# Performance work log

Measured on AMD Instinct MI355X. Metric: run time of the kernel, lower is better.

The kernel has to match this reference:

```python
import jax, jax.numpy as jnp
import numpy as np

D_MODEL = 256
NHEAD = 8
DK = D_MODEL // NHEAD
EDGE_FEAT_DIM = 7
N_NODES = 2048
N_EDGES = 65536
LN_EPS = 1e-5


def _ln(x, g, b):
    mu = jnp.mean(x, axis=-1, keepdims=True)
    var = jnp.mean(jnp.square(x - mu), axis=-1, keepdims=True)
    return (x - mu) * jax.lax.rsqrt(var + LN_EPS) * g + b


def setup_inputs() -> dict:
    key = jax.random.key(0)
    ks = jax.random.split(key, 16)
    d, h2 = D_MODEL, 2 * D_MODEL
    s = 0.02
    inp = {
        "h": jax.random.normal(ks[0], (N_NODES, d), jnp.float32),
        "edge_attr": jax.random.normal(ks[1], (N_EDGES, EDGE_FEAT_DIM), jnp.float32),
        # weights stored as (in, out): y = x @ W + b (matches torch Linear math)
        "Wq": s * jax.random.normal(ks[2], (d, d), jnp.float32),
        "bq": jnp.zeros((d,), jnp.float32),
        "Wk": s * jax.random.normal(ks[3], (d, d), jnp.float32),
        "bk": jnp.zeros((d,), jnp.float32),
        "Wv": s * jax.random.normal(ks[4], (d, d), jnp.float32),
        "bv": jnp.zeros((d,), jnp.float32),
        "Wo": s * jax.random.normal(ks[5], (d, d), jnp.float32),
        "bo": jnp.zeros((d,), jnp.float32),
        "We": s * jax.random.normal(ks[6], (EDGE_FEAT_DIM, NHEAD), jnp.float32),
        "be": jnp.zeros((NHEAD,), jnp.float32),
        "ln1_g": jnp.ones((d,), jnp.float32),
        "ln1_b": jnp.zeros((d,), jnp.float32),
        "fln_g": jnp.ones((d,), jnp.float32),
        "fln_b": jnp.zeros((d,), jnp.float32),
        "W1": s * jax.random.normal(ks[7], (d, h2), jnp.float32),
        "b1": jnp.zeros((h2,), jnp.float32),
        "W2": s * jax.random.normal(ks[8], (h2, d), jnp.float32),
        "b2": jnp.zeros((d,), jnp.float32),
        "edge_index": jax.random.randint(ks[9], (2, N_EDGES), 0, N_NODES, jnp.int64 if jax.config.jax_enable_x64 else jnp.int32),
    }
    return inp


def reference(h, edge_attr, Wq, bq, Wk, bk, Wv, bv, Wo, bo, We, be,
              ln1_g, ln1_b, fln_g, fln_b, W1, b1, W2, b2, edge_index):
    N = h.shape[0]
    res = h
    # edge bias scattered into dense (N, N, H) tensor
    eb = edge_attr @ We + be                                  # (E, H)
    attn_bias = jnp.zeros((N, N, NHEAD), h.dtype).at[edge_index[0], edge_index[1]].set(eb)
    Q = (h @ Wq + bq).reshape(N, NHEAD, DK)
    K = (h @ Wk + bk).reshape(N, NHEAD, DK)
    V = (h @ Wv + bv).reshape(N, NHEAD, DK)
    scores = jnp.einsum('nhd,mhd->nmh', Q, K) / jnp.sqrt(jnp.float32(DK)) + attn_bias
    attn = jax.nn.softmax(scores, axis=1)                     # softmax over keys m
    out = jnp.einsum('nmh,mhd->nhd', attn, V).reshape(N, D_MODEL)
    out = out @ Wo + bo
    h1 = _ln(res + out, ln1_g, ln1_b)
    ffn = jax.nn.gelu(_ln(h1, fln_g, fln_b) @ W1 + b1, approximate=False) @ W2 + b2
    return h1 + ffn
```

## Files before the change

### kernel.cpp

```cpp
#include <hip/hip_runtime.h>
#include <math.h>

#define NN 2048
#define NE 65536
#define DM 256
#define NH 8
#define DKH 32
#define CAP 128
#define TM2 128
#define SPLIT 4

typedef __attribute__((ext_vector_type(8))) short bf16x8;
typedef __attribute__((ext_vector_type(4))) float f32x4;

#define WAVE_LDS_SYNC() __asm__ volatile("s_waitcnt lgkmcnt(0)" ::: "memory")

__device__ __forceinline__ unsigned short f2b(float f) {
    unsigned u = __float_as_uint(f);
    unsigned r = (u + 0x7FFFu + ((u >> 16) & 1u)) >> 16;
    return (unsigned short)r;
}
__device__ __forceinline__ float b2f(unsigned short s) {
    return __uint_as_float(((unsigned)s) << 16);
}

__global__ __launch_bounds__(256) void prep_all_kernel(
    const float* __restrict__ h, const float* __restrict__ Wq,
    const float* __restrict__ Wk, const float* __restrict__ Wv,
    const float* __restrict__ Wo, const float* __restrict__ W1,
    const float* __restrict__ W2, const float* __restrict__ ea,
    const float* __restrict__ We, const float* __restrict__ be,
    const int* __restrict__ ei,
    unsigned short* __restrict__ hb, unsigned short* __restrict__ Wqkvt,
    unsigned short* __restrict__ Wot, unsigned short* __restrict__ W1t,
    unsigned short* __restrict__ W2t, float* __restrict__ eb,
    int* __restrict__ cnt, int* __restrict__ lst)
{
    int b = blockIdx.x;
    if (b < 4096) {
        int i = b * 256 + threadIdx.x;
        if (i < 524288) {
            hb[i] = f2b(h[i]);
        } else if (i < 720896) {
            int j = i - 524288;
            int n = j >> 8, k = j & 255;
            const float* W = (n < 256) ? Wq : (n < 512) ? Wk : Wv;
            Wqkvt[j] = f2b(W[k * 256 + (n & 255)]);
        } else if (i < 786432) {
            int j = i - 720896;
            int n = j >> 8, k = j & 255;
            Wot[j] = f2b(Wo[k * 256 + n]);
        } else if (i < 917504) {
            int j = i - 786432;
            int n = j >> 8, k = j & 255;
            W1t[j] = f2b(W1[(size_t)k * 512 + n]);
        } else {
            int j = i - 917504;
            int n = j >> 9, k = j & 511;
            W2t[j] = f2b(W2[(size_t)k * 256 + n]);
        }
    } else {
        int e = (b - 4096) * 256 + threadIdx.x;
        float acc[NH];
#pragma unroll
        for (int hh = 0; hh < NH; ++hh) acc[hh] = be[hh];
#pragma unroll
        for (int f = 0; f < 7; ++f) {
            float x = ea[e * 7 + f];
#pragma unroll
            for (int hh = 0; hh < NH; ++hh) acc[hh] = fmaf(x, We[f * NH + hh], acc[hh]);
        }
#pragma unroll
        for (int hh = 0; hh < NH; ++hh)
            eb[e * NH + hh] = acc[hh] * 1.44269504088896f;
        int s = ei[e];
        int p = atomicAdd(&cnt[s], 1);
        if (p < CAP) lst[s * CAP + p] = e;
    }
}

__global__ __launch_bounds__(128) void rowprep_kernel(
    const int* __restrict__ ei, const int* __restrict__ cnt,
    const int* __restrict__ lst, int* __restrict__ sortedDest,
    int* __restrict__ sortedE, int* __restrict__ rowOff)
{
    __shared__ int ds[CAP], es[CAP];
    __shared__ int bc[16], off[17];
    int n = blockIdx.x, t = threadIdx.x;
    int c = cnt[n]; if (c > CAP) c = CAP;
    if (t < 16) bc[t] = 0;
    int e = -1, d = -1;
    if (t < c) { e = lst[n * CAP + t]; d = ei[NE + e]; }
    ds[t] = d; es[t] = e;
    __syncthreads();
    bool win = (t < c);
    if (win) {
        for (int j = 0; j < c; ++j)
            if (ds[j] == d && es[j] > e) { win = false; break; }
    }
    int bkt = (d >= 0) ? (d >> 7) : 0;
    int pos = -1;
    if (win) pos = atomicAdd(&bc[bkt], 1);
    __syncthreads();
    if (t == 0) {
        int s = 0;
        for (int i = 0; i < 16; ++i) { off[i] = s; s += bc[i]; }
        off[16] = s;
    }
    __syncthreads();
    if (win) {
        int p = off[bkt] + pos;
        sortedDest[n * CAP + p] = d;
        sortedE[n * CAP + p] = e;
    }
    if (t < 17) rowOff[n * 17 + t] = off[t];
}

template <int EPI, int MT>
__global__ __launch_bounds__(MT * 4) void gemm_bf16(
    const unsigned short* __restrict__ A, const unsigned short* __restrict__ Bt,
    const float* __restrict__ bias0, const float* __restrict__ bias1,
    const float* __restrict__ bias2, const float* __restrict__ resid,
    void* __restrict__ out0, void* __restrict__ out1, void* __restrict__ out2,
    int M, int N, int K)
{
    __shared__ __align__(16) unsigned short As[MT][136];
    __shared__ __align__(16) unsigned short Bs[64][136];
    int tid = threadIdx.x;
    int wv = tid >> 6, l = tid & 63, l15 = l & 15, quad = l >> 4;
    int m0 = blockIdx.y * MT, n0 = blockIdx.x * 64;

    f32x4 acc[4];
#pragma unroll
    for (int i = 0; i < 4; ++i) acc[i] = (f32x4){0.f, 0.f, 0.f, 0.f};

    for (int k0 = 0; k0 < K; k0 += 128) {
        if (MT == 64) {
            int row = tid >> 2, cb = (tid & 3) * 32;
            const unsigned short* ap = A + (size_t)(m0 + row) * K + k0 + cb;
#pragma unroll
            for (int i = 0; i < 4; ++i)
                *(uint4*)&As[row][cb + i * 8] = *(const uint4*)(ap + i * 8);
            const unsigned short* bp = Bt + (size_t)(n0 + row) * K + k0 + cb;
#pragma unroll
            for (int i = 0; i < 4; ++i)
                *(uint4*)&Bs[row][cb + i * 8] = *(const uint4*)(bp + i * 8);
        } else {
            int rowa = tid >> 2, cba = (tid & 3) * 32;
            const unsigned short* ap = A + (size_t)(m0 + rowa) * K + k0 + cba;
#pragma unroll
            for (int i = 0; i < 4; ++i)
                *(uint4*)&As[rowa][cba + i * 8] = *(const uint4*)(ap + i * 8);
            int rowb = tid >> 1, cbb = (tid & 1) * 64;
            const unsigned short* bp = Bt + (size_t)(n0 + rowb) * K + k0 + cbb;
#pragma unroll
            for (int i = 0; i < 8; ++i)
                *(uint4*)&Bs[rowb][cbb + i * 8] = *(const uint4*)(bp + i * 8);
        }
        __syncthreads();
#pragma unroll
        for (int ks = 0; ks < 4; ++ks) {
            bf16x8 a = *(const bf16x8*)&As[wv * 16 + l15][ks * 32 + quad * 8];
#pragma unroll
            for (int nt = 0; nt < 4; ++nt) {
                bf16x8 b = *(const bf16x8*)&Bs[nt * 16 + l15][ks * 32 + quad * 8];
                acc[nt] = __builtin_amdgcn_mfma_f32_16x16x32_bf16(a, b, acc[nt], 0, 0, 0);
            }
        }
        __syncthreads();
    }

#pragma unroll
    for (int nt = 0; nt < 4; ++nt) {
        int colb = n0 + nt * 16;
        if (EPI == 2 && colb >= 512) {
            int n = colb + l15 - 512;
            float bv = bias2[n];
            unsigned short s0 = f2b(acc[nt][0] + bv);
            unsigned short s1 = f2b(acc[nt][1] + bv);
            unsigned short s2 = f2b(acc[nt][2] + bv);
            unsigned short s3 = f2b(acc[nt][3] + bv);
            uint2 pk = { (unsigned)s0 | ((unsigned)s1 << 16),
                         (unsigned)s2 | ((unsigned)s3 << 16) };
            *(uint2*)((unsigned short*)out2 + (size_t)n * NN + m0 + wv * 16 + quad * 4) = pk;
            continue;
        }
#pragma unroll
        for (int r = 0; r < 4; ++r) {
            int row = m0 + wv * 16 + quad * 4 + r;
            int col = colb + l15;
            float v = acc[nt][r];
            if (EPI == 0) {
                v += bias0[col];
                if (resid) v += resid[(size_t)row * N + col];
                ((float*)out0)[(size_t)row * N + col] = v;
            } else if (EPI == 1) {
                v += bias0[col];
                v = 0.5f * v * (1.0f + erff(v * 0.70710678118654752f));
                ((unsigned short*)out0)[(size_t)row * N + col] = f2b(v);
            } else {
                if (col < 256) {
                    v = (v + bias0[col]) * 0.2550348592f;
                    ((unsigned short*)out0)[(size_t)row * 256 + col] = f2b(v);
                } else {
                    v += bias1[col - 256];
                    ((unsigned short*)out1)[(size_t)row * 256 + col - 256] = f2b(v);
                }
            }
        }
    }
}

__global__ __launch_bounds__(256) void attn_mfma(
    const unsigned short* __restrict__ Qb, const unsigned short* __restrict__ Kb,
    const unsigned short* __restrict__ Vt, const float* __restrict__ eb,
    const int* __restrict__ sortedDest, const int* __restrict__ sortedE,
    const int* __restrict__ rowOff,
    float* __restrict__ accD, float* __restrict__ lD)
{
    __shared__ __align__(16) unsigned short Ks[TM2][40];
    __shared__ __align__(16) unsigned short Vs[32][TM2 + 8];
    __shared__ __align__(16) unsigned short Pn[4][16][TM2 + 16];
    __shared__ float ldelta[4][16];
    int h = blockIdx.y, tid = threadIdx.x;
    int wv = tid >> 6, l = tid & 63, l15 = l & 15, quad = l >> 4;
    int n0 = blockIdx.x * 64 + wv * 16;
    int mz = blockIdx.z;

    if (l < 16) ldelta[wv][l] = 0.f;

    bf16x8 aq = *(const bf16x8*)(Qb + (size_t)(n0 + l15) * DM + h * 32 + quad * 8);

    f32x4 oacc[2];
    oacc[0] = (f32x4){0.f, 0.f, 0.f, 0.f};
    oacc[1] = (f32x4){0.f, 0.f, 0.f, 0.f};
    float lacc = 0.f;
    const unsigned short* Vth = Vt + (size_t)h * 32 * NN;

    int r16 = l >> 2, sub = l & 3;
    int frow = n0 + r16;

    for (int t = 0; t < NN / (TM2 * SPLIT); ++t) {
        int m0 = (mz * (NN / SPLIT)) + t * TM2;
        int ti = m0 >> 7;
        {
            int r = tid >> 1, kc = (tid & 1) * 16;
            const unsigned short* ks = Kb + (size_t)(m0 + r) * DM + h * 32 + kc;
            *(uint4*)&Ks[r][kc]     = *(const uint4*)(ks);
            *(uint4*)&Ks[r][kc + 8] = *(const uint4*)(ks + 8);
            int d = tid >> 3, mc = (tid & 7) * 16;
            const unsigned short* vs = Vth + (size_t)d * NN + m0 + mc;
            *(uint4*)&Vs[d][mc]     = *(const uint4*)(vs);
            *(uint4*)&Vs[d][mc + 8] = *(const uint4*)(vs + 8);
        }
        __syncthreads();
#pragma unroll
        for (int mt = 0; mt < TM2 / 16; ++mt) {
            bf16x8 ak = *(const bf16x8*)&Ks[mt * 16 + l15][quad * 8];
            f32x4 s = __builtin_amdgcn_mfma_f32_16x16x32_bf16(
                ak, aq, (f32x4){0.f, 0.f, 0.f, 0.f}, 0, 0, 0);
            float p0 = __builtin_amdgcn_exp2f(s[0]);
            float p1 = __builtin_amdgcn_exp2f(s[1]);
            float p2 = __builtin_amdgcn_exp2f(s[2]);
            float p3 = __builtin_amdgcn_exp2f(s[3]);
            lacc += (p0 + p1) + (p2 + p3);
            unsigned u0 = (unsigned)f2b(p0) | ((unsigned)f2b(p1) << 16);
            unsigned u1 = (unsigned)f2b(p2) | ((unsigned)f2b(p3) << 16);
            *(uint2*)&Pn[wv][l15][mt * 16 + quad * 4] = (uint2){u0, u1};
        }
        WAVE_LDS_SYNC();
        {
            int o0 = rowOff[frow * 17 + ti];
            int o1 = rowOff[frow * 17 + ti + 1];
            for (int idx = o0 + sub; idx < o1; idx += 4) {
                int d = sortedDest[frow * CAP + idx] - m0;
                int e = sortedE[frow * CAP + idx];
                float expb = __builtin_amdgcn_exp2f(eb[e * NH + h]);
                float pold = b2f(Pn[wv][r16][d]);
                Pn[wv][r16][d] = f2b(pold * expb);
                atomicAdd(&ldelta[wv][r16], pold * (expb - 1.0f));
            }
        }
        WAVE_LDS_SYNC();
#pragma unroll
        for (int kc = 0; kc < TM2 / 32; ++kc) {
            bf16x8 ap = *(const bf16x8*)&Pn[wv][l15][kc * 32 + quad * 8];
#pragma unroll
            for (int nt = 0; nt < 2; ++nt) {
                bf16x8 bv = *(const bf16x8*)&Vs[nt * 16 + l15][kc * 32 + quad * 8];
                oacc[nt] = __builtin_amdgcn_mfma_f32_16x16x32_bf16(ap, bv, oacc[nt], 0, 0, 0);
            }
        }
        __syncthreads();
    }

    lacc += __shfl_xor(lacc, 16);
    lacc += __shfl_xor(lacc, 32);
    float* lDp = lD + (size_t)mz * NN * NH;
    if (l < 16)
        lDp[(size_t)(n0 + l) * NH + h] = lacc + ldelta[wv][l];
    float* aDp = accD + (size_t)mz * NN * DM;
#pragma unroll
    for (int nt = 0; nt < 2; ++nt)
#pragma unroll
        for (int r = 0; r < 4; ++r)
            aDp[(size_t)(n0 + quad * 4 + r) * DM + h * 32 + nt * 16 + l15] = oacc[nt][r];
}

__global__ __launch_bounds__(256) void wo_ln_kernel(
    const float* __restrict__ accD, const float* __restrict__ lD,
    const unsigned short* __restrict__ Wot, const float* __restrict__ bo,
    const float* __restrict__ h, const float* __restrict__ g1,
    const float* __restrict__ b1, const float* __restrict__ g2,
    const float* __restrict__ b2, float* __restrict__ H1,
    unsigned short* __restrict__ X2b)
{
    __shared__ float linv[16][8];
    __shared__ __align__(16) unsigned short As[16][264];
    __shared__ __align__(16) unsigned short Bs[256][40];
    __shared__ float Tt[16][264];
    __shared__ unsigned short X2s[16][264];
    int tid = threadIdx.x, m0 = blockIdx.x * 16;
    int wv = tid >> 6, l = tid & 63, l15 = l & 15, quad = l >> 4;

    if (tid < 128) {
        int r = tid >> 3, hh = tid & 7;
        float ls = 0.f;
#pragma unroll
        for (int s = 0; s < SPLIT; ++s)
            ls += lD[(size_t)s * NN * NH + (size_t)(m0 + r) * NH + hh];
        linv[r][hh] = 1.0f / ls;
    }
    __syncthreads();
#pragma unroll
    for (int ch = 0; ch < 16; ++ch) {
        float o = 0.f;
#pragma unroll
        for (int s = 0; s < SPLIT; ++s)
            o += accD[(size_t)s * NN * DM + (size_t)(m0 + ch) * DM + tid];
        As[ch][tid] = f2b(o * linv[ch][tid >> 5]);
    }
    __syncthreads();

    f32x4 acc[4];
#pragma unroll
    for (int i = 0; i < 4; ++i) acc[i] = (f32x4){0.f, 0.f, 0.f, 0.f};

    for (int k0 = 0; k0 < 256; k0 += 32) {
#pragma unroll
        for (int ps = 0; ps < 4; ++ps) {
            int row = ps * 64 + (tid >> 2), kk = (tid & 3) * 8;
            *(uint4*)&Bs[row][kk] = *(const uint4*)(Wot + (size_t)row * 256 + k0 + kk);
        }
        __syncthreads();
        bf16x8 a = *(const bf16x8*)&As[l15][k0 + quad * 8];
#pragma unroll
        for (int nt = 0; nt < 4; ++nt) {
            bf16x8 b = *(const bf16x8*)&Bs[wv * 64 + nt * 16 + l15][quad * 8];
            acc[nt] = __builtin_amdgcn_mfma_f32_16x16x32_bf16(a, b, acc[nt], 0, 0, 0);
        }
        __syncthreads();
    }

#pragma unroll
    for (int nt = 0; nt < 4; ++nt)
#pragma unroll
        for (int r = 0; r < 4; ++r) {
            int row = quad * 4 + r, col = wv * 64 + nt * 16 + l15;
            Tt[row][col] = acc[nt][r] + bo[col] + h[(size_t)(m0 + row) * DM + col];
        }
    __syncthreads();

    int rr = tid >> 4, l16 = tid & 15;
    float x[16];
#pragma unroll
    for (int j = 0; j < 16; ++j) x[j] = Tt[rr][l16 + 16 * j];
    float mu = 0.f;
#pragma unroll
    for (int j = 0; j < 16; ++j) mu += x[j];
#pragma unroll
    for (int off = 1; off < 16; off <<= 1) mu += __shfl_xor(mu, off);
    mu *= (1.0f / 256.0f);
    float var = 0.f;
#pragma unroll
    for (int j = 0; j < 16; ++j) { float d = x[j] - mu; var += d * d; }
#pragma unroll
    for (int off = 1; off < 16; off <<= 1) var += __shfl_xor(var, off);
    float rs = rsqrtf(var * (1.0f / 256.0f) + 1e-5f);
    float y[16]; float mu2 = 0.f;
#pragma unroll
    for (int j = 0; j < 16; ++j) {
        int c = l16 + 16 * j;
        y[j] = (x[j] - mu) * rs * g1[c] + b1[c];
        mu2 += y[j];
    }
#pragma unroll
    for (int off = 1; off < 16; off <<= 1) mu2 += __shfl_xor(mu2, off);
    mu2 *= (1.0f / 256.0f);
    float var2 = 0.f;
#pragma unroll
    for (int j = 0; j < 16; ++j) { float d = y[j] - mu2; var2 += d * d; }
#pragma unroll
    for (int off = 1; off < 16; off <<= 1) var2 += __shfl_xor(var2, off);
    float rs2 = rsqrtf(var2 * (1.0f / 256.0f) + 1e-5f);
#pragma unroll
    for (int j = 0; j < 16; ++j) {
        int c = l16 + 16 * j;
        Tt[rr][c] = y[j];
        X2s[rr][c] = f2b((y[j] - mu2) * rs2 * g2[c] + b2[c]);
    }
    __syncthreads();
#pragma unroll
    for (int ch = 0; ch < 16; ++ch) {
        H1[(size_t)(m0 + ch) * DM + tid] = Tt[ch][tid];
        X2b[(size_t)(m0 + ch) * DM + tid] = X2s[ch][tid];
    }
}

extern "C" void kernel_launch(void* const* d_in, const int* in_sizes, int n_in,
                              void* d_out, int out_size, void* d_ws, size_t ws_size,
                              hipStream_t stream)
{
    const float* h    = (const float*)d_in[0];
    const float* ea   = (const float*)d_in[1];
    const float* Wq   = (const float*)d_in[2];
    const float* bq   = (const float*)d_in[3];
    const float* Wk   = (const float*)d_in[4];
    const float* bk   = (const float*)d_in[5];
    const float* Wv   = (const float*)d_in[6];
    const float* bv   = (const float*)d_in[7];
    const float* Wo   = (const float*)d_in[8];
    const float* bo   = (const float*)d_in[9];
    const float* We   = (const float*)d_in[10];
    const float* be   = (const float*)d_in[11];
    const float* ln1g = (const float*)d_in[12];
    const float* ln1b = (const float*)d_in[13];
    const float* flng = (const float*)d_in[14];
    const float* flnb = (const float*)d_in[15];
    const float* W1   = (const float*)d_in[16];
    const float* b1   = (const float*)d_in[17];
    const float* W2   = (const float*)d_in[18];
    const float* b2   = (const float*)d_in[19];
    const int*   ei   = (const int*)d_in[20];
    float* out = (float*)d_out;

    char* p = (char*)d_ws;
    float* eb   = (float*)p;           p += (size_t)NE * NH * 4;
    int*   cnt  = (int*)p;             p += (size_t)NN * 4;
    int*   lst  = (int*)p;             p += (size_t)NN * CAP * 4;
    int*   sD   = (int*)p;             p += (size_t)NN * CAP * 4;
    int*   sE   = (int*)p;             p += (size_t)NN * CAP * 4;
    int*   rOff = (int*)p;             p += (size_t)NN * 17 * 4;
    unsigned short* hb    = (unsigned short*)p; p += (size_t)NN * DM * 2;
    unsigned short* Wqkvt = (unsigned short*)p; p += (size_t)768 * 256 * 2;
    unsigned short* Wot   = (unsigned short*)p; p += (size_t)256 * 256 * 2;
    unsigned short* W1t   = (unsigned short*)p; p += (size_t)512 * 256 * 2;
    unsigned short* W2t   = (unsigned short*)p; p += (size_t)256 * 512 * 2;
    unsigned short* Qb    = (unsigned short*)p; p += (size_t)NN * DM * 2;
    unsigned short* Kb    = (unsigned short*)p; p += (size_t)NN * DM * 2;
    unsigned short* Vt    = (unsigned short*)p; p += (size_t)NN * DM * 2;
    float* accD = (float*)p;           p += (size_t)SPLIT * NN * DM * 4;
    float* lD   = (float*)p;           p += (size_t)SPLIT * NN * NH * 4;
    float* H1   = (float*)p;           p += (size_t)NN * DM * 4;
    unsigned short* X2b   = (unsigned short*)p; p += (size_t)NN * DM * 2;
    unsigned short* F1b   = (unsigned short*)p; p += (size_t)NN * 512 * 2;

    hipMemsetAsync(cnt, 0, (size_t)NN * 4, stream);
    prep_all_kernel<<<4096 + NE / 256, 256, 0, stream>>>(
        h, Wq, Wk, Wv, Wo, W1, W2, ea, We, be, ei,
        hb, Wqkvt, Wot, W1t, W2t, eb, cnt, lst);
    rowprep_kernel<<<NN, 128, 0, stream>>>(ei, cnt, lst, sD, sE, rOff);

    gemm_bf16<2, 64><<<dim3(768 / 64, NN / 64), 256, 0, stream>>>(
        hb, Wqkvt, bq, bk, bv, nullptr, Qb, Kb, Vt, NN, 768, 256);

    attn_mfma<<<dim3(NN / 64, NH, SPLIT), 256, 0, stream>>>(
        Qb, Kb, Vt, eb, sD, sE, rOff, accD, lD);

    wo_ln_kernel<<<NN / 16, 256, 0, stream>>>(
        accD, lD, Wot, bo, h, ln1g, ln1b, flng, flnb, H1, X2b);

    gemm_bf16<1, 64><<<dim3(512 / 64, NN / 64), 256, 0, stream>>>(
        X2b, W1t, b1, nullptr, nullptr, nullptr, F1b, nullptr, nullptr, NN, 512, 256);
    gemm_bf16<0, 32><<<dim3(256 / 64, NN / 32), 128, 0, stream>>>(
        F1b, W2t, b2, nullptr, nullptr, H1, out, nullptr, nullptr, NN, 256, 512);
}
```

Measured before the change: 171.7 us.

## Fuse h bf16 conversion into QKV GEMM and replace LDS atomics with shuffles

Removes the separate h-to-bf16 conversion from the prep kernel. The QKV GEMM now loads fp32 h directly and packs it to bf16 while staging into LDS, which drops one global write plus re-read and halves the prep grid. In the attention kernel, the per-row edge-bias correction was accumulated with LDS atomics; it now uses a per-lane register sum reduced with cross-lane shuffles. A cheaper round-half-up bf16 pack helper (pk2) replaces round-to-nearest-even in several places, which slightly changes rounding behaviour.

```diff
diff --git a/kernel.cpp b/kernel.cpp
--- a/kernel.cpp
+++ b/kernel.cpp
@@ -23,44 +23,44 @@
 __device__ __forceinline__ float b2f(unsigned short s) {
     return __uint_as_float(((unsigned)s) << 16);
 }
+__device__ __forceinline__ unsigned pk2(float a, float b) {
+    unsigned ua = __float_as_uint(a) + 0x8000u;
+    unsigned ub = __float_as_uint(b) + 0x8000u;
+    return (ua >> 16) | (ub & 0xFFFF0000u);
+}
 
 __global__ __launch_bounds__(256) void prep_all_kernel(
-    const float* __restrict__ h, const float* __restrict__ Wq,
-    const float* __restrict__ Wk, const float* __restrict__ Wv,
-    const float* __restrict__ Wo, const float* __restrict__ W1,
-    const float* __restrict__ W2, const float* __restrict__ ea,
-    const float* __restrict__ We, const float* __restrict__ be,
-    const int* __restrict__ ei,
-    unsigned short* __restrict__ hb, unsigned short* __restrict__ Wqkvt,
-    unsigned short* __restrict__ Wot, unsigned short* __restrict__ W1t,
-    unsigned short* __restrict__ W2t, float* __restrict__ eb,
-    int* __restrict__ cnt, int* __restrict__ lst)
+    const float* __restrict__ Wq, const float* __restrict__ Wk,
+    const float* __restrict__ Wv, const float* __restrict__ Wo,
+    const float* __restrict__ W1, const float* __restrict__ W2,
+    const float* __restrict__ ea, const float* __restrict__ We,
+    const float* __restrict__ be, const int* __restrict__ ei,
+    unsigned short* __restrict__ Wqkvt, unsigned short* __restrict__ Wot,
+    unsigned short* __restrict__ W1t, unsigned short* __restrict__ W2t,
+    float* __restrict__ eb, int* __restrict__ cnt, int* __restrict__ lst)
 {
     int b = blockIdx.x;
-    if (b < 4096) {
+    if (b < 2048) {
         int i = b * 256 + threadIdx.x;
-        if (i < 524288) {
-            hb[i] = f2b(h[i]);
-        } else if (i < 720896) {
-            int j = i - 524288;
-            int n = j >> 8, k = j & 255;
+        if (i < 196608) {
+            int n = i >> 8, k = i & 255;
             const float* W = (n < 256) ? Wq : (n < 512) ? Wk : Wv;
-            Wqkvt[j] = f2b(W[k * 256 + (n & 255)]);
-        } else if (i < 786432) {
-            int j = i - 720896;
+            Wqkvt[i] = f2b(W[k * 256 + (n & 255)]);
+        } else if (i < 262144) {
+            int j = i - 196608;
             int n = j >> 8, k = j & 255;
             Wot[j] = f2b(Wo[k * 256 + n]);
-        } else if (i < 917504) {
-            int j = i - 786432;
+        } else if (i < 393216) {
+            int j = i - 262144;
             int n = j >> 8, k = j & 255;
             W1t[j] = f2b(W1[(size_t)k * 512 + n]);
         } else {
-            int j = i - 917504;
+            int j = i - 393216;
             int n = j >> 9, k = j & 511;
             W2t[j] = f2b(W2[(size_t)k * 256 + n]);
         }
     } else {
-        int e = (b - 4096) * 256 + threadIdx.x;
+        int e = (b - 2048) * 256 + threadIdx.x;
         float acc[NH];
 #pragma unroll
         for (int hh = 0; hh < NH; ++hh) acc[hh] = be[hh];
@@ -116,9 +116,9 @@
     if (t < 17) rowOff[n * 17 + t] = off[t];
 }
 
-template <int EPI, int MT>
+template <int EPI, int MT, int AF32>
 __global__ __launch_bounds__(MT * 4) void gemm_bf16(
-    const unsigned short* __restrict__ A, const unsigned short* __restrict__ Bt,
+    const void* __restrict__ Av, const unsigned short* __restrict__ Bt,
     const float* __restrict__ bias0, const float* __restrict__ bias1,
     const float* __restrict__ bias2, const float* __restrict__ resid,
     void* __restrict__ out0, void* __restrict__ out1, void* __restrict__ out2,
@@ -137,17 +137,31 @@
     for (int k0 = 0; k0 < K; k0 += 128) {
         if (MT == 64) {
             int row = tid >> 2, cb = (tid & 3) * 32;
-            const unsigned short* ap = A + (size_t)(m0 + row) * K + k0 + cb;
-#pragma unroll
-            for (int i = 0; i < 4; ++i)
-                *(uint4*)&As[row][cb + i * 8] = *(const uint4*)(ap + i * 8);
+            if (AF32) {
+                const float* ap = (const float*)Av + (size_t)(m0 + row) * K + k0 + cb;
+#pragma unroll
+                for (int i = 0; i < 4; ++i) {
+                    float4 f0 = *(const float4*)(ap + i * 8);
+                    float4 f1 = *(const float4*)(ap + i * 8 + 4);
+                    uint4 pk = { pk2(f0.x, f0.y), pk2(f0.z, f0.w),
+                                 pk2(f1.x, f1.y), pk2(f1.z, f1.w) };
+                    *(uint4*)&As[row][cb + i * 8] = pk;
+                }
+            } else {
+                const unsigned short* ap =
+                    (const unsigned short*)Av + (size_t)(m0 + row) * K + k0 + cb;
+#pragma unroll
+                for (int i = 0; i < 4; ++i)
+                    *(uint4*)&As[row][cb + i * 8] = *(const uint4*)(ap + i * 8);
+            }
             const unsigned short* bp = Bt + (size_t)(n0 + row) * K + k0 + cb;
 #pragma unroll
             for (int i = 0; i < 4; ++i)
                 *(uint4*)&Bs[row][cb + i * 8] = *(const uint4*)(bp + i * 8);
         } else {
             int rowa = tid >> 2, cba = (tid & 3) * 32;
-            const unsigned short* ap = A + (size_t)(m0 + rowa) * K + k0 + cba;
+            const unsigned short* ap =
+                (const unsigned short*)Av + (size_t)(m0 + rowa) * K + k0 + cba;
 #pragma unroll
             for (int i = 0; i < 4; ++i)
                 *(uint4*)&As[rowa][cba + i * 8] = *(const uint4*)(ap + i * 8);
@@ -176,12 +190,8 @@
         if (EPI == 2 && colb >= 512) {
             int n = colb + l15 - 512;
             float bv = bias2[n];
-            unsigned short s0 = f2b(acc[nt][0] + bv);
-            unsigned short s1 = f2b(acc[nt][1] + bv);
-            unsigned short s2 = f2b(acc[nt][2] + bv);
-            unsigned short s3 = f2b(acc[nt][3] + bv);
-            uint2 pk = { (unsigned)s0 | ((unsigned)s1 << 16),
-                         (unsigned)s2 | ((unsigned)s3 << 16) };
+            uint2 pk = { pk2(acc[nt][0] + bv, acc[nt][1] + bv),
+                         pk2(acc[nt][2] + bv, acc[nt][3] + bv) };
             *(uint2*)((unsigned short*)out2 + (size_t)n * NN + m0 + wv * 16 + quad * 4) = pk;
             continue;
         }
@@ -221,20 +231,18 @@
     __shared__ __align__(16) unsigned short Ks[TM2][40];
     __shared__ __align__(16) unsigned short Vs[32][TM2 + 8];
     __shared__ __align__(16) unsigned short Pn[4][16][TM2 + 16];
-    __shared__ float ldelta[4][16];
     int h = blockIdx.y, tid = threadIdx.x;
     int wv = tid >> 6, l = tid & 63, l15 = l & 15, quad = l >> 4;
     int n0 = blockIdx.x * 64 + wv * 16;
     int mz = blockIdx.z;
 
-    if (l < 16) ldelta[wv][l] = 0.f;
-
     bf16x8 aq = *(const bf16x8*)(Qb + (size_t)(n0 + l15) * DM + h * 32 + quad * 8);
 
     f32x4 oacc[2];
     oacc[0] = (f32x4){0.f, 0.f, 0.f, 0.f};
     oacc[1] = (f32x4){0.f, 0.f, 0.f, 0.f};
     float lacc = 0.f;
+    float dreg = 0.f;
     const unsigned short* Vth = Vt + (size_t)h * 32 * NN;
 
     int r16 = l >> 2, sub = l & 3;
@@ -264,9 +272,8 @@
             float p2 = __builtin_amdgcn_exp2f(s[2]);
             float p3 = __builtin_amdgcn_exp2f(s[3]);
             lacc += (p0 + p1) + (p2 + p3);
-            unsigned u0 = (unsigned)f2b(p0) | ((unsigned)f2b(p1) << 16);
-            unsigned u1 = (unsigned)f2b(p2) | ((unsigned)f2b(p3) << 16);
-            *(uint2*)&Pn[wv][l15][mt * 16 + quad * 4] = (uint2){u0, u1};
+            *(uint2*)&Pn[wv][l15][mt * 16 + quad * 4] =
+                (uint2){pk2(p0, p1), pk2(p2, p3)};
         }
         WAVE_LDS_SYNC();
         {
@@ -278,7 +285,7 @@
                 float expb = __builtin_amdgcn_exp2f(eb[e * NH + h]);
                 float pold = b2f(Pn[wv][r16][d]);
                 Pn[wv][r16][d] = f2b(pold * expb);
-                atomicAdd(&ldelta[wv][r16], pold * (expb - 1.0f));
+                dreg += pold * (expb - 1.0f);
             }
         }
         WAVE_LDS_SYNC();
@@ -296,9 +303,12 @@
 
     lacc += __shfl_xor(lacc, 16);
     lacc += __shfl_xor(lacc, 32);
+    dreg += __shfl_xor(dreg, 1);
+    dreg += __shfl_xor(dreg, 2);
+    float dtot = __shfl(dreg, l15 * 4);
     float* lDp = lD + (size_t)mz * NN * NH;
     if (l < 16)
-        lDp[(size_t)(n0 + l) * NH + h] = lacc + ldelta[wv][l];
+        lDp[(size_t)(n0 + l) * NH + h] = lacc + dtot;
     float* aDp = accD + (size_t)mz * NN * DM;
 #pragma unroll
     for (int nt = 0; nt < 2; ++nt)
@@ -451,7 +461,6 @@
     int*   sD   = (int*)p;             p += (size_t)NN * CAP * 4;
     int*   sE   = (int*)p;             p += (size_t)NN * CAP * 4;
     int*   rOff = (int*)p;             p += (size_t)NN * 17 * 4;
-    unsigned short* hb    = (unsigned short*)p; p += (size_t)NN * DM * 2;
     unsigned short* Wqkvt = (unsigned short*)p; p += (size_t)768 * 256 * 2;
     unsigned short* Wot   = (unsigned short*)p; p += (size_t)256 * 256 * 2;
     unsigned short* W1t   = (unsigned short*)p; p += (size_t)512 * 256 * 2;
@@ -466,13 +475,13 @@
     unsigned short* F1b   = (unsigned short*)p; p += (size_t)NN * 512 * 2;
 
     hipMemsetAsync(cnt, 0, (size_t)NN * 4, stream);
-    prep_all_kernel<<<4096 + NE / 256, 256, 0, stream>>>(
-        h, Wq, Wk, Wv, Wo, W1, W2, ea, We, be, ei,
-        hb, Wqkvt, Wot, W1t, W2t, eb, cnt, lst);
+    prep_all_kernel<<<2048 + NE / 256, 256, 0, stream>>>(
+        Wq, Wk, Wv, Wo, W1, W2, ea, We, be, ei,
+        Wqkvt, Wot, W1t, W2t, eb, cnt, lst);
     rowprep_kernel<<<NN, 128, 0, stream>>>(ei, cnt, lst, sD, sE, rOff);
 
-    gemm_bf16<2, 64><<<dim3(768 / 64, NN / 64), 256, 0, stream>>>(
-        hb, Wqkvt, bq, bk, bv, nullptr, Qb, Kb, Vt, NN, 768, 256);
+    gemm_bf16<2, 64, 1><<<dim3(768 / 64, NN / 64), 256, 0, stream>>>(
+        h, Wqkvt, bq, bk, bv, nullptr, Qb, Kb, Vt, NN, 768, 256);
 
     attn_mfma<<<dim3(NN / 64, NH, SPLIT), 256, 0, stream>>>(
         Qb, Kb, Vt, eb, sD, sE, rOff, accD, lD);
@@ -480,8 +489,8 @@
     wo_ln_kernel<<<NN / 16, 256, 0, stream>>>(
         accD, lD, Wot, bo, h, ln1g, ln1b, flng, flnb, H1, X2b);
 
-    gemm_bf16<1, 64><<<dim3(512 / 64, NN / 64), 256, 0, stream>>>(
+    gemm_bf16<1, 64, 0><<<dim3(512 / 64, NN / 64), 256, 0, stream>>>(
         X2b, W1t, b1, nullptr, nullptr, nullptr, F1b, nullptr, nullptr, NN, 512, 256);
-    gemm_bf16<0, 32><<<dim3(256 / 64, NN / 32), 128, 0, stream>>>(
+    gemm_bf16<0, 32, 0><<<dim3(256 / 64, NN / 32), 128, 0, stream>>>(
         F1b, W2t, b2, nullptr, nullptr, H1, out, nullptr, nullptr, NN, 256, 512);
 }
```

Measured after the change: 171.1 us. Within noise of the previous version (-0.4%).
